# Kernel optimization log

Hardware: AMD Instinct MI355X
Metric: run time of the kernel (lower is better)

The kernel has to match this reference:

```python
import jax, jax.numpy as jnp
import numpy as np

V, C, T_BLK, H, L = 65, 512, 256, 8, 8
HS = C // H
EPS = 1e-5


def _ln(x, g, b):
    m = jnp.mean(x, axis=-1, keepdims=True)
    v = jnp.mean((x - m) ** 2, axis=-1, keepdims=True)
    return (x - m) * jax.lax.rsqrt(v + EPS) * g + b


def setup_inputs() -> dict:
    key = jax.random.key(0)
    ks = jax.random.split(key, 16)
    B, T = 64, 256
    idx = jax.random.randint(ks[0], (B, T), 0, V)
    targets = jax.random.randint(ks[1], (B, T), 0, V)
    n = lambda k, shape, s: (jax.random.normal(k, shape, dtype=jnp.float32) * s)
    return {
        "idx": idx,
        "targets": targets,
        "tok_emb": n(ks[2], (V, C), 0.02),
        "pos_emb": n(ks[3], (T_BLK, C), 0.02),
        "ln1_g": jnp.ones((L, C), jnp.float32),
        "ln1_b": jnp.zeros((L, C), jnp.float32),
        "wq": n(ks[4], (L, C, C), (2.0 / C) ** 0.5),
        "wk": n(ks[5], (L, C, C), (2.0 / C) ** 0.5),
        "wv": n(ks[6], (L, C, C), (2.0 / C) ** 0.5),
        "wo": n(ks[7], (L, C, C), (2.0 / C) ** 0.5),
        "bo": jnp.zeros((L, C), jnp.float32),
        "ln2_g": jnp.ones((L, C), jnp.float32),
        "ln2_b": jnp.zeros((L, C), jnp.float32),
        "w1": n(ks[8], (L, C, 4 * C), (2.0 / C) ** 0.5),
        "b1": jnp.zeros((L, 4 * C), jnp.float32),
        "w2": n(ks[9], (L, 4 * C, C), (2.0 / (4 * C)) ** 0.5),
        "b2": jnp.zeros((L, C), jnp.float32),
        "lnf_g": jnp.ones((C,), jnp.float32),
        "lnf_b": jnp.zeros((C,), jnp.float32),
        "lm_w": n(ks[10], (C, V), (2.0 / C) ** 0.5),
        "lm_b": jnp.zeros((V,), jnp.float32),
    }


def _gpt_forward(tok_emb, pos_emb, ln1_g, ln1_b, wq, wk, wv, wo, bo,
                 ln2_g, ln2_b, w1, b1, w2, b2, lnf_g, lnf_b, lm_w, lm_b,
                 idx, targets):
    B, T = idx.shape
    x = tok_emb[idx] + pos_emb[:T]  # [B,T,C]
    causal = jnp.tril(jnp.ones((T, T), bool))
    scale = float(C) ** -0.5  # NOTE: scaled by n_embd, not head_size (faithful)
    for l in range(L):
        h = _ln(x, ln1_g[l], ln1_b[l])
        q = (h @ wq[l]).reshape(B, T, H, HS)
        k = (h @ wk[l]).reshape(B, T, H, HS)
        v = (h @ wv[l]).reshape(B, T, H, HS)
        scores = jnp.einsum('bthd,bshd->bhts', q, k) * scale
        scores = jnp.where(causal, scores, -jnp.inf)
        w = jax.nn.softmax(scores, axis=-1)
        attn = jnp.einsum('bhts,bshd->bthd', w, v).reshape(B, T, C)
        x = x + attn @ wo[l] + bo[l]
        h2 = _ln(x, ln2_g[l], ln2_b[l])
        x = x + jax.nn.relu(h2 @ w1[l] + b1[l]) @ w2[l] + b2[l]
    x = _ln(x, lnf_g, lnf_b)
    logits = (x @ lm_w + lm_b).reshape(B * T, V)
    logp = jax.nn.log_softmax(logits, axis=-1)
    tgt = targets.reshape(B * T)
    loss = -jnp.mean(jnp.take_along_axis(logp, tgt[:, None], axis=-1))
    return logits, loss


def reference(idx, targets, tok_emb, pos_emb, ln1_g, ln1_b, wq, wk, wv, wo, bo,
              ln2_g, ln2_b, w1, b1, w2, b2, lnf_g, lnf_b, lm_w, lm_b):
    return _gpt_forward(tok_emb, pos_emb, ln1_g, ln1_b, wq, wk, wv, wo, bo,
                        ln2_g, ln2_b, w1, b1, w2, b2, lnf_g, lnf_b, lm_w, lm_b,
                        idx, targets)
```

## Files before the change

### kernel.cpp

```cpp
#include <hip/hip_runtime.h>
#include <math.h>

#define V_SZ   65
#define C_DIM  512
#define T_SEQ  256
#define H_N    8
#define HS_D   64
#define L_N    8
#define N_TOK  16384
#define LN_EPS 1e-5f
#define SM_SCALE 0.044194173824159216f

typedef unsigned short ushortT;
typedef __attribute__((ext_vector_type(8))) short    short8;
typedef __attribute__((ext_vector_type(8))) ushortT  ushort8;
typedef __attribute__((ext_vector_type(4))) float    f32x4;

typedef __attribute__((address_space(3))) unsigned int        lds_uint;
typedef const __attribute__((address_space(1))) unsigned int  glob_uint;

__device__ inline ushortT f2bf(float f) {
    unsigned int u = __float_as_uint(f);
    u = (u + 0x7fffu + ((u >> 16) & 1u)) >> 16;
    return (ushortT)u;
}
__device__ inline float bf2f(ushortT u) {
    return __uint_as_float(((unsigned int)u) << 16);
}

__global__ void embed_kernel(const int* __restrict__ idx,
                             const float* __restrict__ tok,
                             const float* __restrict__ pos,
                             ushortT* __restrict__ x) {
    int i = blockIdx.x * blockDim.x + threadIdx.x;
    const int NC8 = N_TOK * C_DIM / 8;
    if (i >= NC8) return;
    int c8 = i % (C_DIM / 8);
    int n  = i / (C_DIM / 8);
    int t  = n % T_SEQ;
    int tk = idx[n];
    const float4* ta = (const float4*)&tok[(size_t)tk * C_DIM + c8 * 8];
    const float4* pa = (const float4*)&pos[(size_t)t  * C_DIM + c8 * 8];
    float4 a0 = ta[0], a1 = ta[1], p0 = pa[0], p1 = pa[1];
    ushort8 r;
    r[0] = f2bf(a0.x + p0.x); r[1] = f2bf(a0.y + p0.y);
    r[2] = f2bf(a0.z + p0.z); r[3] = f2bf(a0.w + p0.w);
    r[4] = f2bf(a1.x + p1.x); r[5] = f2bf(a1.y + p1.y);
    r[6] = f2bf(a1.z + p1.z); r[7] = f2bf(a1.w + p1.w);
    *(ushort8*)&x[(size_t)i * 8] = r;
}

__global__ __launch_bounds__(256) void tcast_kernel(const float* __restrict__ src,
                                                    ushortT* __restrict__ dst,
                                                    int K, int N) {
    __shared__ float tile[32][33];
    size_t lo = (size_t)blockIdx.z * K * N;
    int n0 = blockIdx.x * 32, k0 = blockIdx.y * 32;
    int tx = threadIdx.x & 31, ty = threadIdx.x >> 5;
    #pragma unroll
    for (int s = 0; s < 4; s++) {
        int kk = ty + s * 8;
        tile[kk][tx] = src[lo + (size_t)(k0 + kk) * N + n0 + tx];
    }
    __syncthreads();
    #pragma unroll
    for (int s = 0; s < 4; s++) {
        int nn = ty + s * 8;
        dst[lo + (size_t)(n0 + nn) * K + k0 + tx] = f2bf(tile[tx][nn]);
    }
}

__global__ __launch_bounds__(256) void lmcast_kernel(const float* __restrict__ w,
                                                     ushortT* __restrict__ dst) {
    int n = blockIdx.x;
    for (int k = threadIdx.x; k < C_DIM; k += 256)
        dst[(size_t)n * C_DIM + k] = (n < V_SZ) ? f2bf(w[(size_t)k * V_SZ + n]) : (ushortT)0;
}

__global__ __launch_bounds__(256) void ln_kernel(const ushortT* __restrict__ in,
                                                 const float* __restrict__ g,
                                                 const float* __restrict__ b,
                                                 ushortT* __restrict__ outv) {
    int wave = threadIdx.x >> 6;
    int lane = threadIdx.x & 63;
    int row  = blockIdx.x * 4 + wave;
    ushort8 raw = *(const ushort8*)&in[(size_t)row * C_DIM + lane * 8];
    float v[8];
    #pragma unroll
    for (int k = 0; k < 8; k++) v[k] = bf2f(raw[k]);
    float s = 0.f;
    #pragma unroll
    for (int k = 0; k < 8; k++) s += v[k];
    #pragma unroll
    for (int m = 32; m >= 1; m >>= 1) s += __shfl_xor(s, m, 64);
    float mean = s * (1.0f / C_DIM);
    float vs = 0.f;
    #pragma unroll
    for (int k = 0; k < 8; k++) { float d = v[k] - mean; vs += d * d; }
    #pragma unroll
    for (int m = 32; m >= 1; m >>= 1) vs += __shfl_xor(vs, m, 64);
    float rstd = rsqrtf(vs * (1.0f / C_DIM) + LN_EPS);
    float gv[8], bv[8];
    *(float4*)&gv[0] = *(const float4*)&g[lane * 8];
    *(float4*)&gv[4] = *(const float4*)&g[lane * 8 + 4];
    *(float4*)&bv[0] = *(const float4*)&b[lane * 8];
    *(float4*)&bv[4] = *(const float4*)&b[lane * 8 + 4];
    ushort8 pack;
    #pragma unroll
    for (int k = 0; k < 8; k++) pack[k] = f2bf((v[k] - mean) * rstd * gv[k] + bv[k]);
    *(ushort8*)&outv[(size_t)row * C_DIM + lane * 8] = pack;
}

template<int EPI>
__device__ __forceinline__ void gemm_core(const ushortT* __restrict__ A,
                                          const ushortT* __restrict__ Bt,
                                          const float* __restrict__ bias,
                                          void* __restrict__ outp,
                                          int N, int K,
                                          int mBase, int nBase) {
    __shared__ __align__(16) ushortT As[128 * 32];
    __shared__ __align__(16) ushortT Bs[128 * 32];
    const int tid = threadIdx.x;
    const int w = tid >> 6, lane = tid & 63;
    const int wr = w >> 1, wc = w & 1;
    const int l15 = lane & 15, lg = lane >> 4;
    const int srow = (lane >> 2);
    const int sslot = lane & 3;

    f32x4 acc[4][4];
    #pragma unroll
    for (int i = 0; i < 4; i++)
        #pragma unroll
        for (int j = 0; j < 4; j++)
            acc[i][j] = {0.f, 0.f, 0.f, 0.f};

    for (int k0 = 0; k0 < K; k0 += 32) {
        #pragma unroll
        for (int t = 0; t < 2; t++) {
            int r = w * 32 + t * 16 + srow;
            int ks = sslot ^ ((r >> 1) & 3);
            const ushortT* ga = &A[(size_t)(mBase + r) * K + k0 + ks * 8];
            __builtin_amdgcn_global_load_lds((glob_uint*)ga,
                (lds_uint*)&As[(w * 32 + t * 16) * 32], 16, 0, 0);
            const ushortT* gb = &Bt[(size_t)(nBase + r) * K + k0 + ks * 8];
            __builtin_amdgcn_global_load_lds((glob_uint*)gb,
                (lds_uint*)&Bs[(w * 32 + t * 16) * 32], 16, 0, 0);
        }
        __syncthreads();
        short8 af[4], bfr[4];
        #pragma unroll
        for (int i = 0; i < 4; i++) {
            int r = wr * 64 + i * 16 + l15;
            int cb = (lg * 16) ^ (((r >> 1) & 3) << 4);
            af[i] = *(const short8*)((const char*)As + r * 64 + cb);
        }
        #pragma unroll
        for (int j = 0; j < 4; j++) {
            int r = wc * 64 + j * 16 + l15;
            int cb = (lg * 16) ^ (((r >> 1) & 3) << 4);
            bfr[j] = *(const short8*)((const char*)Bs + r * 64 + cb);
        }
        #pragma unroll
        for (int i = 0; i < 4; i++)
            #pragma unroll
            for (int j = 0; j < 4; j++)
                acc[i][j] = __builtin_amdgcn_mfma_f32_16x16x32_bf16(af[i], bfr[j], acc[i][j], 0, 0, 0);
        __syncthreads();
    }

    int lr = lg * 4;
    #pragma unroll
    for (int i = 0; i < 4; i++) {
        #pragma unroll
        for (int j = 0; j < 4; j++) {
            int col = nBase + wc * 64 + j * 16 + l15;
            if (EPI == 4 && col >= V_SZ) continue;
            #pragma unroll
            for (int q = 0; q < 4; q++) {
                size_t row = (size_t)(mBase + wr * 64 + i * 16 + lr + q);
                float vv = acc[i][j][q];
                if (EPI >= 2) vv += bias[col];
                if (EPI == 2) vv = fmaxf(vv, 0.f);
                if (EPI == 1)      ((ushortT*)outp)[row * N + col] = f2bf(vv);
                else if (EPI == 2) ((ushortT*)outp)[row * N + col] = f2bf(vv);
                else               ((float*)outp)[row * V_SZ + col] = vv;
            }
        }
    }
}

template<int EPI>
__global__ __launch_bounds__(256, 2) void gemm_bf16(const ushortT* __restrict__ A,
                                                    const ushortT* __restrict__ Bt,
                                                    const float* __restrict__ bias,
                                                    void* __restrict__ outp,
                                                    int N, int K) {
    gemm_core<EPI>(A, Bt, bias, outp, N, K, blockIdx.x * 128, blockIdx.y * 128);
}

__global__ __launch_bounds__(256, 2) void gemm_qkv(const ushortT* __restrict__ A,
                                                   const ushortT* __restrict__ bq,
                                                   const ushortT* __restrict__ bk,
                                                   const ushortT* __restrict__ bv,
                                                   ushortT* __restrict__ oq,
                                                   ushortT* __restrict__ ok,
                                                   ushortT* __restrict__ ov,
                                                   int N, int K) {
    const ushortT* Bt = (blockIdx.z == 0) ? bq : (blockIdx.z == 1) ? bk : bv;
    ushortT*       o  = (blockIdx.z == 0) ? oq : (blockIdx.z == 1) ? ok : ov;
    gemm_core<1>(A, Bt, nullptr, o, N, K, blockIdx.x * 128, blockIdx.y * 128);
}

__global__ __launch_bounds__(256, 2) void gemm_w1_wide(const ushortT* __restrict__ A,
                                                       const ushortT* __restrict__ Bt,
                                                       const float* __restrict__ bias,
                                                       ushortT* __restrict__ outp,
                                                       int N, int K) {
    __shared__ __align__(16) ushortT As[128 * 32];
    __shared__ __align__(16) ushortT Bs[256 * 32];
    const int tid = threadIdx.x;
    const int w = tid >> 6, lane = tid & 63;
    const int wr = w >> 1, wc = w & 1;
    const int l15 = lane & 15, lg = lane >> 4;
    const int mBase = blockIdx.x * 128, nBase = blockIdx.y * 256;

    f32x4 acc[4][8];
    #pragma unroll
    for (int i = 0; i < 4; i++)
        #pragma unroll
        for (int j = 0; j < 8; j++)
            acc[i][j] = {0.f, 0.f, 0.f, 0.f};

    for (int k0 = 0; k0 < K; k0 += 32) {
        #pragma unroll
        for (int i = 0; i < 2; i++) {
            int c = w * 64 + i * 256 + lane;
            int r = c >> 2;
            int ks = (c & 3) ^ ((r >> 1) & 3);
            const ushortT* ga = &A[(size_t)(mBase + r) * K + k0 + ks * 8];
            __builtin_amdgcn_global_load_lds((glob_uint*)ga,
                (lds_uint*)&As[(w * 64 + i * 256) * 8], 16, 0, 0);
        }
        #pragma unroll
        for (int i = 0; i < 4; i++) {
            int c = w * 64 + i * 256 + lane;
            int r = c >> 2;
            int ks = (c & 3) ^ ((r >> 1) & 3);
            const ushortT* gb = &Bt[(size_t)(nBase + r) * K + k0 + ks * 8];
            __builtin_amdgcn_global_load_lds((glob_uint*)gb,
                (lds_uint*)&Bs[(w * 64 + i * 256) * 8], 16, 0, 0);
        }
        __syncthreads();
        short8 af[4], bfr[8];
        #pragma unroll
        for (int i = 0; i < 4; i++) {
            int r = wr * 64 + i * 16 + l15;
            int cb = (lg * 16) ^ (((r >> 1) & 3) << 4);
            af[i] = *(const short8*)((const char*)As + r * 64 + cb);
        }
        #pragma unroll
        for (int j = 0; j < 8; j++) {
            int r = wc * 128 + j * 16 + l15;
            int cb = (lg * 16) ^ (((r >> 1) & 3) << 4);
            bfr[j] = *(const short8*)((const char*)Bs + r * 64 + cb);
        }
        #pragma unroll
        for (int i = 0; i < 4; i++)
            #pragma unroll
            for (int j = 0; j < 8; j++)
                acc[i][j] = __builtin_amdgcn_mfma_f32_16x16x32_bf16(af[i], bfr[j], acc[i][j], 0, 0, 0);
        __syncthreads();
    }

    int lr = lg * 4;
    #pragma unroll
    for (int i = 0; i < 4; i++) {
        #pragma unroll
        for (int j = 0; j < 8; j++) {
            int col = nBase + wc * 128 + j * 16 + l15;
            #pragma unroll
            for (int q = 0; q < 4; q++) {
                size_t row = (size_t)(mBase + wr * 64 + i * 16 + lr + q);
                float vv = acc[i][j][q] + bias[col];
                vv = fmaxf(vv, 0.f);
                outp[row * N + col] = f2bf(vv);
            }
        }
    }
}

__global__ __launch_bounds__(256, 2) void gemm_k64_res(const ushortT* __restrict__ A,
                                                       const ushortT* __restrict__ Bt,
                                                       const float* __restrict__ bias,
                                                       const ushortT* __restrict__ res,
                                                       ushortT* __restrict__ outp,
                                                       int N, int K) {
    __shared__ __align__(16) ushortT As[2][128 * 64];
    __shared__ __align__(16) ushortT Bs[2][128 * 64];
    const int tid = threadIdx.x;
    const int w = tid >> 6, lane = tid & 63;
    const int wr = w >> 1, wc = w & 1;
    const int l15 = lane & 15, lg = lane >> 4;
    const int mBase = blockIdx.x * 128, nBase = blockIdx.y * 128;
    const int NT = K >> 6;
    const int srow = lane >> 3;
    const int sgran = lane & 7;

    f32x4 acc[4][4];
    #pragma unroll
    for (int i = 0; i < 4; i++)
        #pragma unroll
        for (int j = 0; j < 4; j++)
            acc[i][j] = {0.f, 0.f, 0.f, 0.f};

    auto stage = [&](int buf, int k0) {
        #pragma unroll
        for (int t = 0; t < 4; t++) {
            int r = w * 32 + t * 8 + srow;
            int gl = sgran ^ (r & 7);
            const ushortT* ga = &A[(size_t)(mBase + r) * K + k0 + gl * 8];
            __builtin_amdgcn_global_load_lds((glob_uint*)ga,
                (lds_uint*)&As[buf][(w * 32 + t * 8) * 64], 16, 0, 0);
            const ushortT* gb = &Bt[(size_t)(nBase + r) * K + k0 + gl * 8];
            __builtin_amdgcn_global_load_lds((glob_uint*)gb,
                (lds_uint*)&Bs[buf][(w * 32 + t * 8) * 64], 16, 0, 0);
        }
    };

    stage(0, 0);
    int cur = 0;
    for (int t = 0; t < NT; t++) {
        asm volatile("s_waitcnt vmcnt(0)" ::: "memory");
        __builtin_amdgcn_s_barrier();
        __builtin_amdgcn_sched_barrier(0);
        if (t + 1 < NT) stage(cur ^ 1, (t + 1) * 64);

        const char* as = (const char*)&As[cur][0];
        const char* bs = (const char*)&Bs[cur][0];
        short8 af[2][4], bfr[2][4];
        #pragma unroll
        for (int i = 0; i < 4; i++) {
            int r = wr * 64 + i * 16 + l15;
            #pragma unroll
            for (int kk = 0; kk < 2; kk++) {
                int g = (kk * 4 + lg) ^ (r & 7);
                af[kk][i] = *(const short8*)(as + r * 128 + g * 16);
            }
        }
        #pragma unroll
        for (int j = 0; j < 4; j++) {
            int r = wc * 64 + j * 16 + l15;
            #pragma unroll
            for (int kk = 0; kk < 2; kk++) {
                int g = (kk * 4 + lg) ^ (r & 7);
                bfr[kk][j] = *(const short8*)(bs + r * 128 + g * 16);
            }
        }
        __builtin_amdgcn_s_setprio(1);
        #pragma unroll
        for (int kk = 0; kk < 2; kk++)
            #pragma unroll
            for (int i = 0; i < 4; i++)
                #pragma unroll
                for (int j = 0; j < 4; j++)
                    acc[i][j] = __builtin_amdgcn_mfma_f32_16x16x32_bf16(af[kk][i], bfr[kk][j], acc[i][j], 0, 0, 0);
        __builtin_amdgcn_s_setprio(0);
        asm volatile("s_waitcnt lgkmcnt(0)" ::: "memory");
        cur ^= 1;
    }

    int lr = lg * 4;
    #pragma unroll
    for (int i = 0; i < 4; i++) {
        #pragma unroll
        for (int j = 0; j < 4; j++) {
            int col = nBase + wc * 64 + j * 16 + l15;
            #pragma unroll
            for (int q = 0; q < 4; q++) {
                size_t row = (size_t)(mBase + wr * 64 + i * 16 + lr + q);
                float vv = acc[i][j][q] + bias[col] + bf2f(res[row * N + col]);
                outp[row * N + col] = f2bf(vv);
            }
        }
    }
}

__global__ __launch_bounds__(256) void attn_kernel(const ushortT* __restrict__ qp,
                                                   const ushortT* __restrict__ kp,
                                                   const ushortT* __restrict__ vp,
                                                   ushortT* __restrict__ att) {
    __shared__ ushortT K_lds[T_SEQ][72];
    __shared__ ushortT Vt_lds[HS_D][264];
    __shared__ ushortT P_lds[4][16][72];
    int bh = blockIdx.x;
    int b = bh >> 3, h = bh & 7;
    int tid = threadIdx.x;
    int w = tid >> 6, lane = tid & 63;
    const size_t rowbase = (size_t)b * T_SEQ * C_DIM + (size_t)h * HS_D;
    int l15 = lane & 15, lg = lane >> 4;

    #pragma unroll
    for (int it = 0; it < 8; it++) {
        int f = tid + it * 256;
        int r = f >> 3, c8 = f & 7;
        ushort8 kb = *(const ushort8*)&kp[rowbase + (size_t)r * C_DIM + c8 * 8];
        *(ushort8*)&K_lds[r][c8 * 8] = kb;
        ushort8 vb = *(const ushort8*)&vp[rowbase + (size_t)r * C_DIM + c8 * 8];
        #pragma unroll
        for (int e = 0; e < 8; e++) Vt_lds[c8 * 8 + e][r] = vb[e];
    }

    short8 qf[4][2];
    #pragma unroll
    for (int i = 0; i < 4; i++) {
        int grow = 16 * (4 * i + w) + l15;
        #pragma unroll
        for (int kk = 0; kk < 2; kk++)
            qf[i][kk] = *(const short8*)&qp[rowbase + (size_t)grow * C_DIM + kk * 32 + lg * 8];
    }
    __syncthreads();

    f32x4 acc_o[4][4];
    float mrun[4][4], lrun[4][4];
    #pragma unroll
    for (int i = 0; i < 4; i++) {
        #pragma unroll
        for (int j = 0; j < 4; j++) acc_o[i][j] = {0.f, 0.f, 0.f, 0.f};
        #pragma unroll
        for (int q = 0; q < 4; q++) { mrun[i][q] = -1e30f; lrun[i][q] = 0.f; }
    }

    const int UJ[10] = {0,0,0,0, 1,1,1, 2,2, 3};
    const int UI[10] = {0,1,2,3, 1,2,3, 2,3, 3};

    auto qk = [&](int jt, int i, f32x4* dst) {
        #pragma unroll
        for (int j_ = 0; j_ < 4; j_++) dst[j_] = {0.f, 0.f, 0.f, 0.f};
        #pragma unroll
        for (int j_ = 0; j_ < 4; j_++)
            #pragma unroll
            for (int kk = 0; kk < 2; kk++) {
                short8 kf = *(const short8*)&K_lds[jt * 64 + j_ * 16 + l15][kk * 32 + lg * 8];
                dst[j_] = __builtin_amdgcn_mfma_f32_16x16x32_bf16(qf[i][kk], kf, dst[j_], 0, 0, 0);
            }
    };

    f32x4 sCur[4];
    qk(UJ[0], UI[0], sCur);

    #pragma unroll
    for (int u = 0; u < 10; u++) {
        const int jt = UJ[u], i = UI[u];
        f32x4 sNxt[4];
        if (u < 9) qk(UJ[u + 1], UI[u + 1], sNxt);

        float sv[4][4];
        #pragma unroll
        for (int j_ = 0; j_ < 4; j_++) {
            int colg = jt * 64 + j_ * 16 + l15;
            #pragma unroll
            for (int q = 0; q < 4; q++) {
                int rowg = 16 * (4 * i + w) + lg * 4 + q;
                float s = sCur[j_][q] * SM_SCALE;
                sv[j_][q] = (i == jt && colg > rowg) ? -1e30f : s;
            }
        }
        #pragma unroll
        for (int q = 0; q < 4; q++) {
            float mx = fmaxf(fmaxf(sv[0][q], sv[1][q]), fmaxf(sv[2][q], sv[3][q]));
            #pragma unroll
            for (int msk = 1; msk <= 8; msk <<= 1) mx = fmaxf(mx, __shfl_xor(mx, msk, 64));
            float mold = mrun[i][q];
            float mnew = fmaxf(mold, mx);
            float corr = __expf(mold - mnew);
            mrun[i][q] = mnew;
            float ps = 0.f;
            #pragma unroll
            for (int j_ = 0; j_ < 4; j_++) {
                float pe = __expf(sv[j_][q] - mnew);
                ps += pe;
                P_lds[w][lg * 4 + q][j_ * 16 + l15] = f2bf(pe);
            }
            lrun[i][q] = lrun[i][q] * corr + ps;
            #pragma unroll
            for (int dj = 0; dj < 4; dj++) acc_o[i][dj][q] *= corr;
        }
        short8 pa[2];
        #pragma unroll
        for (int kk = 0; kk < 2; kk++)
            pa[kk] = *(const short8*)&P_lds[w][l15][kk * 32 + lg * 8];
        #pragma unroll
        for (int dj = 0; dj < 4; dj++)
            #pragma unroll
            for (int kk = 0; kk < 2; kk++) {
                short8 vf = *(const short8*)&Vt_lds[dj * 16 + l15][jt * 64 + kk * 32 + lg * 8];
                acc_o[i][dj] = __builtin_amdgcn_mfma_f32_16x16x32_bf16(pa[kk], vf, acc_o[i][dj], 0, 0, 0);
            }
        if (u < 9) {
            #pragma unroll
            for (int j_ = 0; j_ < 4; j_++) sCur[j_] = sNxt[j_];
        }
    }

    #pragma unroll
    for (int i = 0; i < 4; i++) {
        float inv[4];
        #pragma unroll
        for (int q = 0; q < 4; q++) {
            float ls = lrun[i][q];
            #pragma unroll
            for (int msk = 1; msk <= 8; msk <<= 1) ls += __shfl_xor(ls, msk, 64);
            inv[q] = 1.0f / ls;
        }
        #pragma unroll
        for (int dj = 0; dj < 4; dj++) {
            int colg = dj * 16 + l15;
            #pragma unroll
            for (int q = 0; q < 4; q++) {
                int rowg = 16 * (4 * i + w) + lg * 4 + q;
                att[rowbase + (size_t)rowg * C_DIM + colg] = f2bf(acc_o[i][dj][q] * inv[q]);
            }
        }
    }
}

__global__ __launch_bounds__(256) void rowloss_kernel(const float* __restrict__ logits,
                                                      const int* __restrict__ tgt,
                                                      float* __restrict__ rl) {
    int wave = threadIdx.x >> 6, lane = threadIdx.x & 63;
    int n = blockIdx.x * 4 + wave;
    const float* l = logits + (size_t)n * V_SZ;
    float v0 = l[lane];
    float v1 = (lane == 0) ? l[64] : -1e30f;
    float m = fmaxf(v0, v1);
    #pragma unroll
    for (int s = 32; s >= 1; s >>= 1) m = fmaxf(m, __shfl_xor(m, s, 64));
    float e = __expf(v0 - m) + ((lane == 0) ? __expf(v1 - m) : 0.f);
    #pragma unroll
    for (int s = 32; s >= 1; s >>= 1) e += __shfl_xor(e, s, 64);
    if (lane == 0) {
        float lp = l[tgt[n]] - m - logf(e);
        rl[n] = -lp;
    }
}

__global__ __launch_bounds__(256) void reduce_loss_kernel(const float* __restrict__ rl,
                                                          float* __restrict__ out_loss) {
    __shared__ float sdata[256];
    float s = 0.f;
    for (int i = threadIdx.x; i < N_TOK; i += 256) s += rl[i];
    sdata[threadIdx.x] = s;
    __syncthreads();
    for (int st = 128; st > 0; st >>= 1) {
        if (threadIdx.x < st) sdata[threadIdx.x] += sdata[threadIdx.x + st];
        __syncthreads();
    }
    if (threadIdx.x == 0) out_loss[0] = sdata[0] * (1.0f / N_TOK);
}

extern "C" void kernel_launch(void* const* d_in, const int* in_sizes, int n_in,
                              void* d_out, int out_size, void* d_ws, size_t ws_size,
                              hipStream_t stream) {
    const int*   idx     = (const int*)d_in[0];
    const int*   targets = (const int*)d_in[1];
    const float* tok_emb = (const float*)d_in[2];
    const float* pos_emb = (const float*)d_in[3];
    const float* ln1_g   = (const float*)d_in[4];
    const float* ln1_b   = (const float*)d_in[5];
    const float* wq      = (const float*)d_in[6];
    const float* wk      = (const float*)d_in[7];
    const float* wv      = (const float*)d_in[8];
    const float* wo      = (const float*)d_in[9];
    const float* bo      = (const float*)d_in[10];
    const float* ln2_g   = (const float*)d_in[11];
    const float* ln2_b   = (const float*)d_in[12];
    const float* w1      = (const float*)d_in[13];
    const float* b1      = (const float*)d_in[14];
    const float* w2      = (const float*)d_in[15];
    const float* b2      = (const float*)d_in[16];
    const float* lnf_g   = (const float*)d_in[17];
    const float* lnf_b   = (const float*)d_in[18];
    const float* lm_w    = (const float*)d_in[19];
    const float* lm_b    = (const float*)d_in[20];

    float* out = (float*)d_out;
    char*  ws  = (char*)d_ws;
    const size_t MB = 1024ull * 1024ull;
    ushortT* x_bf  = (ushortT*)(ws);
    ushortT* h_bf  = (ushortT*)(ws + 32 * MB);
    ushortT* q_bf  = (ushortT*)(ws + 48 * MB);
    ushortT* k_bf  = (ushortT*)(ws + 64 * MB);
    ushortT* v_bf  = (ushortT*)(ws + 80 * MB);
    ushortT* att_bf= (ushortT*)(ws + 112 * MB);
    ushortT* ff1_bf= (ushortT*)(ws + 48 * MB);
    ushortT* wqT   = (ushortT*)(ws + 128 * MB);
    ushortT* wkT   = (ushortT*)(ws + 132 * MB);
    ushortT* wvT   = (ushortT*)(ws + 136 * MB);
    ushortT* woT   = (ushortT*)(ws + 140 * MB);
    ushortT* w1T   = (ushortT*)(ws + 144 * MB);
    ushortT* w2T   = (ushortT*)(ws + 160 * MB);
    float*   rl    = (float*)(ws + 176 * MB);
    ushortT* lmT   = (ushortT*)(ws + 177 * MB);

    {
        dim3 gCC(C_DIM / 32, C_DIM / 32, L_N);
        tcast_kernel<<<gCC, 256, 0, stream>>>(wq, wqT, C_DIM, C_DIM);
        tcast_kernel<<<gCC, 256, 0, stream>>>(wk, wkT, C_DIM, C_DIM);
        tcast_kernel<<<gCC, 256, 0, stream>>>(wv, wvT, C_DIM, C_DIM);
        tcast_kernel<<<gCC, 256, 0, stream>>>(wo, woT, C_DIM, C_DIM);
        dim3 g1(4 * C_DIM / 32, C_DIM / 32, L_N);
        tcast_kernel<<<g1, 256, 0, stream>>>(w1, w1T, C_DIM, 4 * C_DIM);
        dim3 g2(C_DIM / 32, 4 * C_DIM / 32, L_N);
        tcast_kernel<<<g2, 256, 0, stream>>>(w2, w2T, 4 * C_DIM, C_DIM);
        lmcast_kernel<<<128, 256, 0, stream>>>(lm_w, lmT);
    }

    embed_kernel<<<(N_TOK * C_DIM / 8 + 255) / 256, 256, 0, stream>>>(idx, tok_emb, pos_emb, x_bf);

    dim3 gemmCC(N_TOK / 128, C_DIM / 128);
    dim3 gemmW1(N_TOK / 128, 4 * C_DIM / 256);
    dim3 gemmQKV(N_TOK / 128, C_DIM / 128, 3);

    for (int l = 0; l < L_N; l++) {
        const ushortT* wqT_l = wqT + (size_t)l * C_DIM * C_DIM;
        const ushortT* wkT_l = wkT + (size_t)l * C_DIM * C_DIM;
        const ushortT* wvT_l = wvT + (size_t)l * C_DIM * C_DIM;
        const ushortT* woT_l = woT + (size_t)l * C_DIM * C_DIM;
        const ushortT* w1T_l = w1T + (size_t)l * C_DIM * 4 * C_DIM;
        const ushortT* w2T_l = w2T + (size_t)l * C_DIM * 4 * C_DIM;

        ln_kernel<<<N_TOK / 4, 256, 0, stream>>>(x_bf, ln1_g + l * C_DIM, ln1_b + l * C_DIM, h_bf);
        gemm_qkv<<<gemmQKV, 256, 0, stream>>>(h_bf, wqT_l, wkT_l, wvT_l, q_bf, k_bf, v_bf, C_DIM, C_DIM);
        attn_kernel<<<64 * H_N, 256, 0, stream>>>(q_bf, k_bf, v_bf, att_bf);
        gemm_k64_res<<<gemmCC, 256, 0, stream>>>(att_bf, woT_l, bo + l * C_DIM, x_bf, x_bf, C_DIM, C_DIM);
        ln_kernel<<<N_TOK / 4, 256, 0, stream>>>(x_bf, ln2_g + l * C_DIM, ln2_b + l * C_DIM, h_bf);
        gemm_w1_wide<<<gemmW1, 256, 0, stream>>>(h_bf, w1T_l, b1 + (size_t)l * 4 * C_DIM, ff1_bf, 4 * C_DIM, C_DIM);
        gemm_k64_res<<<gemmCC, 256, 0, stream>>>(ff1_bf, w2T_l, b2 + l * C_DIM, x_bf, x_bf, C_DIM, 4 * C_DIM);
    }

    ln_kernel<<<N_TOK / 4, 256, 0, stream>>>(x_bf, lnf_g, lnf_b, h_bf);
    gemm_bf16<4><<<dim3(N_TOK / 128, 1), 256, 0, stream>>>(h_bf, lmT, lm_b, out, V_SZ, C_DIM);

    rowloss_kernel<<<N_TOK / 4, 256, 0, stream>>>(out, targets, rl);
    reduce_loss_kernel<<<1, 256, 0, stream>>>(rl, out + (size_t)N_TOK * V_SZ);
}
```

Baseline: 1.549 ms.

## Replace W1 GEMM with barrier-free per-wave double-buffered kernel

The FFN up-projection GEMM now has each wave load its own private 64x32 A and B tiles into per-wave double-buffered LDS and sync only via vmcnt waits. This removes the block-wide __syncthreads and overlaps the next tile's global loads with MFMA work. Each wave loads all of its operands itself, so A and B tiles are no longer shared across waves. That raises global/L2 traffic, and the block tile shrinks from 128x256 to 128x128 with twice the grid.

```diff
diff --git a/kernel.cpp b/kernel.cpp
--- a/kernel.cpp
+++ b/kernel.cpp
@@ -211,76 +211,92 @@
     gemm_core<1>(A, Bt, nullptr, o, N, K, blockIdx.x * 128, blockIdx.y * 128);
 }
 
-__global__ __launch_bounds__(256, 2) void gemm_w1_wide(const ushortT* __restrict__ A,
-                                                       const ushortT* __restrict__ Bt,
-                                                       const float* __restrict__ bias,
-                                                       ushortT* __restrict__ outp,
-                                                       int N, int K) {
-    __shared__ __align__(16) ushortT As[128 * 32];
-    __shared__ __align__(16) ushortT Bs[256 * 32];
+__global__ __launch_bounds__(256, 2) void gemm_nobar(const ushortT* __restrict__ A,
+                                                     const ushortT* __restrict__ Bt,
+                                                     const float* __restrict__ bias,
+                                                     ushortT* __restrict__ outp,
+                                                     int N, int K) {
+    __shared__ __align__(16) ushortT Abuf[4][2][64 * 32];
+    __shared__ __align__(16) ushortT Bbuf[4][2][64 * 32];
     const int tid = threadIdx.x;
     const int w = tid >> 6, lane = tid & 63;
     const int wr = w >> 1, wc = w & 1;
     const int l15 = lane & 15, lg = lane >> 4;
-    const int mBase = blockIdx.x * 128, nBase = blockIdx.y * 256;
-
-    f32x4 acc[4][8];
+    const int aRow0 = blockIdx.x * 128 + wr * 64;
+    const int bRow0 = blockIdx.y * 128 + wc * 64;
+    const int NT = K >> 5;
+
+    f32x4 acc[4][4];
     #pragma unroll
     for (int i = 0; i < 4; i++)
         #pragma unroll
-        for (int j = 0; j < 8; j++)
+        for (int j = 0; j < 4; j++)
             acc[i][j] = {0.f, 0.f, 0.f, 0.f};
 
-    for (int k0 = 0; k0 < K; k0 += 32) {
-        #pragma unroll
-        for (int i = 0; i < 2; i++) {
-            int c = w * 64 + i * 256 + lane;
+    auto stage = [&](int buf, int k0) {
+        #pragma unroll
+        for (int i = 0; i < 4; i++) {
+            int c = i * 64 + lane;
             int r = c >> 2;
             int ks = (c & 3) ^ ((r >> 1) & 3);
-            const ushortT* ga = &A[(size_t)(mBase + r) * K + k0 + ks * 8];
+            const ushortT* ga = &A[(size_t)(aRow0 + r) * K + k0 + ks * 8];
             __builtin_amdgcn_global_load_lds((glob_uint*)ga,
-                (lds_uint*)&As[(w * 64 + i * 256) * 8], 16, 0, 0);
+                (lds_uint*)&Abuf[w][buf][i * 512], 16, 0, 0);
         }
         #pragma unroll
         for (int i = 0; i < 4; i++) {
-            int c = w * 64 + i * 256 + lane;
+            int c = i * 64 + lane;
             int r = c >> 2;
             int ks = (c & 3) ^ ((r >> 1) & 3);
-            const ushortT* gb = &Bt[(size_t)(nBase + r) * K + k0 + ks * 8];
+            const ushortT* gb = &Bt[(size_t)(bRow0 + r) * K + k0 + ks * 8];
             __builtin_amdgcn_global_load_lds((glob_uint*)gb,
-                (lds_uint*)&Bs[(w * 64 + i * 256) * 8], 16, 0, 0);
-        }
-        __syncthreads();
-        short8 af[4], bfr[8];
+                (lds_uint*)&Bbuf[w][buf][i * 512], 16, 0, 0);
+        }
+    };
+
+    stage(0, 0);
+    int cur = 0;
+    for (int t = 0; t < NT; t++) {
+        if (t + 1 < NT) {
+            stage(cur ^ 1, (t + 1) * 32);
+            asm volatile("s_waitcnt vmcnt(8)" ::: "memory");
+        } else {
+            asm volatile("s_waitcnt vmcnt(0)" ::: "memory");
+        }
+        const char* as = (const char*)&Abuf[w][cur][0];
+        const char* bs = (const char*)&Bbuf[w][cur][0];
+        short8 af[4], bfr[4];
         #pragma unroll
         for (int i = 0; i < 4; i++) {
-            int r = wr * 64 + i * 16 + l15;
+            int r = i * 16 + l15;
             int cb = (lg * 16) ^ (((r >> 1) & 3) << 4);
-            af[i] = *(const short8*)((const char*)As + r * 64 + cb);
-        }
-        #pragma unroll
-        for (int j = 0; j < 8; j++) {
-            int r = wc * 128 + j * 16 + l15;
+            af[i] = *(const short8*)(as + r * 64 + cb);
+        }
+        #pragma unroll
+        for (int j = 0; j < 4; j++) {
+            int r = j * 16 + l15;
             int cb = (lg * 16) ^ (((r >> 1) & 3) << 4);
-            bfr[j] = *(const short8*)((const char*)Bs + r * 64 + cb);
-        }
+            bfr[j] = *(const short8*)(bs + r * 64 + cb);
+        }
+        __builtin_amdgcn_s_setprio(1);
         #pragma unroll
         for (int i = 0; i < 4; i++)
             #pragma unroll
-            for (int j = 0; j < 8; j++)
+            for (int j = 0; j < 4; j++)
                 acc[i][j] = __builtin_amdgcn_mfma_f32_16x16x32_bf16(af[i], bfr[j], acc[i][j], 0, 0, 0);
-        __syncthreads();
+        __builtin_amdgcn_s_setprio(0);
+        cur ^= 1;
     }
 
     int lr = lg * 4;
     #pragma unroll
     for (int i = 0; i < 4; i++) {
         #pragma unroll
-        for (int j = 0; j < 8; j++) {
-            int col = nBase + wc * 128 + j * 16 + l15;
+        for (int j = 0; j < 4; j++) {
+            int col = bRow0 + j * 16 + l15;
             #pragma unroll
             for (int q = 0; q < 4; q++) {
-                size_t row = (size_t)(mBase + wr * 64 + i * 16 + lr + q);
+                size_t row = (size_t)(aRow0 + i * 16 + lr + q);
                 float vv = acc[i][j][q] + bias[col];
                 vv = fmaxf(vv, 0.f);
                 outp[row * N + col] = f2bf(vv);
@@ -618,7 +634,7 @@
     embed_kernel<<<(N_TOK * C_DIM / 8 + 255) / 256, 256, 0, stream>>>(idx, tok_emb, pos_emb, x_bf);
 
     dim3 gemmCC(N_TOK / 128, C_DIM / 128);
-    dim3 gemmW1(N_TOK / 128, 4 * C_DIM / 256);
+    dim3 gemmW1(N_TOK / 128, 4 * C_DIM / 128);
     dim3 gemmQKV(N_TOK / 128, C_DIM / 128, 3);
 
     for (int l = 0; l < L_N; l++) {
@@ -634,7 +650,7 @@
         attn_kernel<<<64 * H_N, 256, 0, stream>>>(q_bf, k_bf, v_bf, att_bf);
         gemm_k64_res<<<gemmCC, 256, 0, stream>>>(att_bf, woT_l, bo + l * C_DIM, x_bf, x_bf, C_DIM, C_DIM);
         ln_kernel<<<N_TOK / 4, 256, 0, stream>>>(x_bf, ln2_g + l * C_DIM, ln2_b + l * C_DIM, h_bf);
-        gemm_w1_wide<<<gemmW1, 256, 0, stream>>>(h_bf, w1T_l, b1 + (size_t)l * 4 * C_DIM, ff1_bf, 4 * C_DIM, C_DIM);
+        gemm_nobar<<<gemmW1, 256, 0, stream>>>(h_bf, w1T_l, b1 + (size_t)l * 4 * C_DIM, ff1_bf, 4 * C_DIM, C_DIM);
         gemm_k64_res<<<gemmCC, 256, 0, stream>>>(ff1_bf, w2T_l, b2 + l * C_DIM, x_bf, x_bf, C_DIM, 4 * C_DIM);
     }
 
```

Measured after the change: 1.667 ms. +7.6%, slower.
